# Kernel tuning notes

Hardware: AMD Instinct MI355X
Metric: run time of the kernel (lower is better)

## Reference

```python
import jax, jax.numpy as jnp
import numpy as np
import math

C = 512          # in_planes
H = 8            # num_heads
D = C // H       # head_dim = 64
EPS = 1e-12      # torch F.normalize eps


def _l2norm(x):
    # F.normalize(x, dim=-1): x / max(||x||_2, eps)
    n = jnp.sqrt(jnp.sum(x * x, axis=-1, keepdims=True))
    return x / jnp.maximum(n, EPS)


def setup_inputs() -> dict:
    key = jax.random.key(0)
    ks = jax.random.split(key, 8)
    q = jax.random.normal(ks[0], (8, 8, 256, C), dtype=jnp.float32)
    kv = jax.random.normal(ks[1], (8, 8, 512, C), dtype=jnp.float32)
    s = 0.02
    Wq = jax.random.normal(ks[2], (C, C), dtype=jnp.float32) * s
    bq = jax.random.normal(ks[3], (C,), dtype=jnp.float32) * s
    Wkv = jax.random.normal(ks[4], (2 * C, C), dtype=jnp.float32) * s
    bkv = jax.random.normal(ks[5], (2 * C,), dtype=jnp.float32) * s
    Wm = jax.random.normal(ks[6], (C, C), dtype=jnp.float32) * s
    bm = jax.random.normal(ks[7], (C,), dtype=jnp.float32) * s
    return {"q": q, "kv": kv, "Wq": Wq, "bq": bq, "Wkv": Wkv, "bkv": bkv, "Wm": Wm, "bm": bm}


def reference(q, kv, Wq, bq, Wkv, bkv, Wm, bm):
    b, t, lq, c = q.shape
    lk = kv.shape[2]
    shortcut = q

    # Q projection -> (b,t,h,lq,d), L2-normalized over d
    qh = (q @ Wq.T + bq).reshape(b, t, lq, H, D)
    qh = _l2norm(jnp.moveaxis(qh, 3, 2))  # (b,t,h,lq,d)

    # KV projection -> (b,t,2h,lk,d); first H heads = k, last H = v
    kvh = (kv @ Wkv.T + bkv).reshape(b, t, lk, 2 * H, D)
    kvh = jnp.moveaxis(kvh, 3, 2)          # (b,t,2h,lk,d)
    kh = _l2norm(kvh[:, :, :H])            # (b,t,h,lk,d)
    vh = _l2norm(kvh[:, :, H:])            # (b,t,h,lk,d)

    # cosine attention
    att = jnp.einsum('bthqd,bthkd->bthqk', qh, kh) / math.sqrt(D)
    att = jax.nn.softmax(att, axis=-1)
    x = jnp.einsum('bthqk,bthkd->bthqd', att, vh)  # (b,t,h,lq,d)

    # merge heads, output projection, residual
    x = jnp.moveaxis(x, 2, 3).reshape(b, t, lq, c)
    return x @ Wm.T + bm + shortcut
```

## Files before the change

### kernel.cpp

```cpp
#include <hip/hip_runtime.h>
#include <hip/hip_bf16.h>

using bf = __bf16;
typedef __attribute__((ext_vector_type(8))) __bf16 bf16x8;
typedef __attribute__((ext_vector_type(4))) float f32x4;

#define MFMA(a, b, c) __builtin_amdgcn_mfma_f32_16x16x32_bf16((a), (b), (c), 0, 0, 0)
#define GLL16(g, s)                                                         \
    __builtin_amdgcn_global_load_lds(                                       \
        (const __attribute__((address_space(1))) void*)(g),                 \
        (__attribute__((address_space(3))) void*)(s), 16, 0, 0)

static __device__ __forceinline__ void cvt_one(const float* __restrict__ s,
                                               bf* __restrict__ d, int i)
{
    const f32x4 a = ((const f32x4*)s)[2 * i];
    const f32x4 b = ((const f32x4*)s)[2 * i + 1];
    bf16x8 r;
#pragma unroll
    for (int k = 0; k < 4; ++k) { r[k] = (bf)a[k]; r[4 + k] = (bf)b[k]; }
    ((bf16x8*)d)[i] = r;
}

__global__ __launch_bounds__(256) void cvt2(const float* __restrict__ s1, bf* __restrict__ d1, int n1,
                                            const float* __restrict__ s2, bf* __restrict__ d2, int n2)
{
    int i = blockIdx.x * 256 + threadIdx.x;
    if (i < n1) { cvt_one(s1, d1, i); return; }
    i -= n1;
    if (i < n2) cvt_one(s2, d2, i);
}

__global__ __launch_bounds__(256) void cvt3(const float* __restrict__ s1, bf* __restrict__ d1, int n1,
                                            const float* __restrict__ s2, bf* __restrict__ d2, int n2,
                                            const float* __restrict__ s3, bf* __restrict__ d3, int n3)
{
    int i = blockIdx.x * 256 + threadIdx.x;
    if (i < n1) { cvt_one(s1, d1, i); return; }
    i -= n1;
    if (i < n2) { cvt_one(s2, d2, i); return; }
    i -= n2;
    if (i < n3) cvt_one(s3, d3, i);
}

template <int EPI, int GH, int LGR>
__global__ __launch_bounds__(256) void gemm128(
    const bf* __restrict__ A, const bf* __restrict__ W,
    const float* __restrict__ bias, const float* __restrict__ res,
    void* __restrict__ Cout, int M, int N, int K)
{
    __shared__ __attribute__((aligned(16))) bf As[128 * 32];
    __shared__ __attribute__((aligned(16))) bf Bs[128 * 32];

    const int lane = threadIdx.x & 63;
    const int wave = threadIdx.x >> 6;
    const int lm = lane & 15;
    const int quad = lane >> 4;
    const int row0 = blockIdx.x * 128, col0 = blockIdx.y * 128;
    const int wrow = (wave >> 1) * 64, wcol = (wave & 1) * 64;

    const int sr = lane >> 2;
    const int sc = (lane & 3) * 8;
    const bf* Ag = A + (size_t)(row0 + wave * 32 + sr) * K + sc;
    const bf* Wg = W + (size_t)(col0 + wave * 32 + sr) * K + sc;
    bf* AsW = As + wave * 1024;
    bf* BsW = Bs + wave * 1024;

    f32x4 acc[4][4] = {};

    for (int k0 = 0; k0 < K; k0 += 32) {
        GLL16(Ag + k0, AsW);
        GLL16(Ag + (size_t)16 * K + k0, AsW + 512);
        GLL16(Wg + k0, BsW);
        GLL16(Wg + (size_t)16 * K + k0, BsW + 512);
        __syncthreads();

        bf16x8 a[4], b[4];
#pragma unroll
        for (int i = 0; i < 4; ++i)
            a[i] = *(const bf16x8*)(As + (wrow + i * 16 + lm) * 32 + quad * 8);
#pragma unroll
        for (int j = 0; j < 4; ++j)
            b[j] = *(const bf16x8*)(Bs + (wcol + j * 16 + lm) * 32 + quad * 8);
#pragma unroll
        for (int i = 0; i < 4; ++i)
#pragma unroll
            for (int j = 0; j < 4; ++j)
                acc[i][j] = MFMA(a[i], b[j], acc[i][j]);
        __syncthreads();
    }

    float bv[4];
#pragma unroll
    for (int j = 0; j < 4; ++j) bv[j] = bias[col0 + wcol + j * 16 + lm];

    if (EPI == 0) {
        bf* C = (bf*)Cout;
        const int g = (col0 + wcol) >> 6;
#pragma unroll
        for (int i = 0; i < 4; ++i) {
#pragma unroll
            for (int rg = 0; rg < 4; ++rg) {
                float v[4];
                float ss = 0.f;
#pragma unroll
                for (int j = 0; j < 4; ++j) {
                    const float x = acc[i][j][rg] + bv[j];
                    v[j] = x;
                    ss += x * x;
                }
                ss += __shfl_xor(ss, 1, 64);
                ss += __shfl_xor(ss, 2, 64);
                ss += __shfl_xor(ss, 4, 64);
                ss += __shfl_xor(ss, 8, 64);
                const float inv = 1.0f / fmaxf(sqrtf(ss), 1e-12f);
                const int row = row0 + wrow + i * 16 + quad * 4 + rg;
                const int bt = row >> LGR;
                const int rl = row & ((1 << LGR) - 1);
                bf* Cr = C + (((size_t)(bt * GH + g) << LGR) + rl) * 64;
#pragma unroll
                for (int j = 0; j < 4; ++j)
                    Cr[j * 16 + lm] = (bf)(v[j] * inv);
            }
        }
    } else {
        float* C = (float*)Cout;
#pragma unroll
        for (int i = 0; i < 4; ++i) {
#pragma unroll
            for (int rg = 0; rg < 4; ++rg) {
                const int row = row0 + wrow + i * 16 + quad * 4 + rg;
#pragma unroll
                for (int j = 0; j < 4; ++j) {
                    const size_t idx = (size_t)row * N + col0 + wcol + j * 16 + lm;
                    C[idx] = acc[i][j][rg] + bv[j] + res[idx];
                }
            }
        }
    }
}

template <int GH, int LGR>
__global__ __launch_bounds__(512, 2) void gemm256(
    const bf* __restrict__ A, const bf* __restrict__ W,
    const float* __restrict__ bias, bf* __restrict__ C,
    int M, int N, int K)
{
    extern __shared__ __attribute__((aligned(16))) char smem[];
    char* Asm = smem;
    char* Bsm = smem + 65536;

    const int tid = threadIdx.x;
    const int lane = tid & 63;
    const int lm = lane & 15;
    const int quad = lane >> 4;
    const int wave = tid >> 6;
    const int wm = wave >> 2;
    const int wn = wave & 3;
    const int row0 = blockIdx.x * 256, col0 = blockIdx.y * 256;
    const int NT = K >> 6;

    const int trow = tid >> 3;
    const int tslot = (tid & 7) ^ (trow & 7);
    const bf* Ath = A + (size_t)(row0 + trow) * K + tslot * 8;
    const bf* Wth = W + (size_t)(col0 + trow) * K + tslot * 8;

    const char* aBase = Asm + wm * 16384 + lm * 128;
    const char* bBase = Bsm + (wn >> 1) * 16384 + ((wn & 1) * 64 + lm) * 128;
    const int skz0 = ((quad ^ (lm & 7)) << 4);
    const int skz1 = (((4 + quad) ^ (lm & 7)) << 4);

    f32x4 acc[8][4] = {};

    auto stA = [&](int kt) {
        const int bo = (kt & 1) * 32768;
#pragma unroll
        for (int h = 0; h < 2; ++h)
#pragma unroll
            for (int s = 0; s < 2; ++s)
                GLL16(Ath + (size_t)(h * 128 + s * 64) * K + kt * 64,
                      Asm + bo + h * 16384 + s * 8192 + tid * 16);
    };
    auto stB = [&](int kt) {
        const int bo = (kt & 1) * 32768;
#pragma unroll
        for (int h = 0; h < 2; ++h)
#pragma unroll
            for (int s = 0; s < 2; ++s)
                GLL16(Wth + (size_t)(h * 128 + s * 64) * K + kt * 64,
                      Bsm + bo + h * 16384 + s * 8192 + tid * 16);
    };

#define LOADA(bo, mh, kk)                                                     \
    _Pragma("unroll")                                                         \
    for (int mm = 0; mm < 4; ++mm)                                            \
        a[mm] = *(const bf16x8*)(aBase + (bo) + ((mh) * 4 + mm) * 2048        \
                                 + ((kk) ? skz1 : skz0));
#define LOADB(bo, kk)                                                         \
    _Pragma("unroll")                                                         \
    for (int j = 0; j < 4; ++j)                                               \
        b[j] = *(const bf16x8*)(bBase + (bo) + j * 2048                       \
                                + ((kk) ? skz1 : skz0));
#define PH_OPEN()                                                             \
    __builtin_amdgcn_s_barrier();                                             \
    asm volatile("s_waitcnt lgkmcnt(0)" ::: "memory");                        \
    __builtin_amdgcn_s_setprio(1)
#define MM16(mh)                                                              \
    _Pragma("unroll")                                                         \
    for (int mm = 0; mm < 4; ++mm)                                            \
        _Pragma("unroll")                                                     \
        for (int j = 0; j < 4; ++j)                                           \
            acc[(mh) * 4 + mm][j] = MFMA(a[mm], b[j], acc[(mh) * 4 + mm][j]);
#define PH_CLOSE()                                                            \
    __builtin_amdgcn_s_setprio(0);                                            \
    __builtin_amdgcn_s_barrier()

    stB(0); stA(0); stB(1);
    asm volatile("s_waitcnt vmcnt(4)" ::: "memory");
    __builtin_amdgcn_s_barrier();

    for (int it = 0; it < NT; it += 2) {
        const int more = (it + 2 < NT);
        bf16x8 a[4], b[4];

        LOADA(0, 0, 0) LOADB(0, 0) stA(it + 1);
        PH_OPEN(); MM16(0) PH_CLOSE();

        LOADA(0, 1, 0)
        PH_OPEN(); MM16(1) PH_CLOSE();

        LOADA(0, 0, 1) LOADB(0, 1)
        PH_OPEN(); MM16(0) PH_CLOSE();

        LOADA(0, 1, 1) if (more) stB(it + 2);
        PH_OPEN(); MM16(1)
        __builtin_amdgcn_s_setprio(0);
        if (more) { asm volatile("s_waitcnt vmcnt(4)" ::: "memory"); }
        else      { asm volatile("s_waitcnt vmcnt(0)" ::: "memory"); }
        __builtin_amdgcn_s_barrier();

        LOADA(32768, 0, 0) LOADB(32768, 0) if (more) stA(it + 2);
        PH_OPEN(); MM16(0) PH_CLOSE();

        LOADA(32768, 1, 0)
        PH_OPEN(); MM16(1) PH_CLOSE();

        LOADA(32768, 0, 1) LOADB(32768, 1)
        PH_OPEN(); MM16(0) PH_CLOSE();

        LOADA(32768, 1, 1) if (more) stB(it + 3);
        PH_OPEN(); MM16(1)
        __builtin_amdgcn_s_setprio(0);
        if (more) { asm volatile("s_waitcnt vmcnt(4)" ::: "memory"); }
        __builtin_amdgcn_s_barrier();
    }
#undef LOADA
#undef LOADB
#undef PH_OPEN
#undef MM16
#undef PH_CLOSE

    float bv[4];
#pragma unroll
    for (int j = 0; j < 4; ++j) bv[j] = bias[col0 + wn * 64 + j * 16 + lm];
    const int g = (col0 + wn * 64) >> 6;
#pragma unroll
    for (int m = 0; m < 8; ++m) {
#pragma unroll
        for (int rg = 0; rg < 4; ++rg) {
            float v[4];
            float ss = 0.f;
#pragma unroll
            for (int j = 0; j < 4; ++j) {
                const float x = acc[m][j][rg] + bv[j];
                v[j] = x;
                ss += x * x;
            }
            ss += __shfl_xor(ss, 1, 64);
            ss += __shfl_xor(ss, 2, 64);
            ss += __shfl_xor(ss, 4, 64);
            ss += __shfl_xor(ss, 8, 64);
            const float inv = 1.0f / fmaxf(sqrtf(ss), 1e-12f);
            const int row = row0 + wm * 128 + m * 16 + quad * 4 + rg;
            const int bt = row >> LGR;
            const int rl = row & ((1 << LGR) - 1);
            bf* Cr = C + (((size_t)(bt * GH + g) << LGR) + rl) * 64;
#pragma unroll
            for (int j = 0; j < 4; ++j)
                Cr[j * 16 + lm] = (bf)(v[j] * inv);
        }
    }
}

__global__ __launch_bounds__(256, 4) void attn(
    const bf* __restrict__ qn, const bf* __restrict__ kvn, bf* __restrict__ X)
{
    __shared__ __attribute__((aligned(16))) bf Kt[128 * 72];
    __shared__ __attribute__((aligned(16))) bf Vt[64 * 136];
    __shared__ __attribute__((aligned(16))) bf Ps[4][16 * 40];

    const int qb = blockIdx.x >> 9;
    const int rb = blockIdx.x & 511;
    const int bt = rb >> 3;
    const int h = rb & 7;
    const int tid = threadIdx.x;
    const int lane = tid & 63;
    const int wave = tid >> 6;
    const int lm = lane & 15;
    const int quad = lane >> 4;

    const bf* qh = qn + ((size_t)(bt * 8 + h) * 256 + qb * 128) * 64;
    const bf* kh = kvn + (size_t)(bt * 16 + h) * 512 * 64;
    const bf* vh = kvn + (size_t)(bt * 16 + 8 + h) * 512 * 64;

    const int srow = tid >> 1;
    const int sseg = (tid & 1) * 32;

    f32x4 o[2][4] = {};
    float sum[2][4] = {};
    bf* Pw = &Ps[wave][0];

    for (int t = 0; t < 4; ++t) {
        {
            const bf* kr = kh + (size_t)(t * 128 + srow) * 64 + sseg;
            bf* kd = Kt + srow * 72 + sseg;
#pragma unroll
            for (int j = 0; j < 4; ++j)
                *(bf16x8*)(kd + j * 8) = *(const bf16x8*)(kr + j * 8);

            const bf* vr = vh + (size_t)(t * 128 + srow) * 64 + sseg;
            bf16x8 vv[4];
#pragma unroll
            for (int j = 0; j < 4; ++j) vv[j] = *(const bf16x8*)(vr + j * 8);
#pragma unroll
            for (int j = 0; j < 4; ++j)
#pragma unroll
                for (int e = 0; e < 8; ++e)
                    Vt[(sseg + j * 8 + e) * 136 + srow] = vv[j][e];
        }
        __syncthreads();

#pragma unroll
        for (int c = 0; c < 2; ++c) {
            const int r0 = wave * 32 + c * 16;
            const bf* qp = qh + (size_t)(r0 + lm) * 64 + quad * 8;
            const bf16x8 a0 = *(const bf16x8*)qp;
            const bf16x8 a1 = *(const bf16x8*)(qp + 32);

            f32x4 s[8];
#pragma unroll
            for (int nt = 0; nt < 8; ++nt) {
                const bf16x8 k0 = *(const bf16x8*)(&Kt[(nt * 16 + lm) * 72 + quad * 8]);
                const bf16x8 k1 = *(const bf16x8*)(&Kt[(nt * 16 + lm) * 72 + 32 + quad * 8]);
                f32x4 z = {};
                z = MFMA(a0, k0, z);
                s[nt] = MFMA(a1, k1, z);
            }

            for (int ntp = 0; ntp < 4; ++ntp) {
#pragma unroll
                for (int tt = 0; tt < 2; ++tt)
#pragma unroll
                    for (int rr = 0; rr < 4; ++rr) {
                        const float e = __expf(s[ntp * 2 + tt][rr] * 0.125f);
                        sum[c][rr] += e;
                        Pw[(quad * 4 + rr) * 40 + tt * 16 + lm] = (bf)e;
                    }
                const bf16x8 ap = *(const bf16x8*)(&Pw[lm * 40 + quad * 8]);
#pragma unroll
                for (int dt = 0; dt < 4; ++dt) {
                    const bf16x8 bv = *(const bf16x8*)(&Vt[(dt * 16 + lm) * 136 + ntp * 32 + quad * 8]);
                    o[c][dt] = MFMA(ap, bv, o[c][dt]);
                }
            }
        }
        __syncthreads();
    }

#pragma unroll
    for (int c = 0; c < 2; ++c) {
        float inv[4];
#pragma unroll
        for (int rr = 0; rr < 4; ++rr) {
            float sm = sum[c][rr];
            sm += __shfl_xor(sm, 1, 64);
            sm += __shfl_xor(sm, 2, 64);
            sm += __shfl_xor(sm, 4, 64);
            sm += __shfl_xor(sm, 8, 64);
            inv[rr] = 1.0f / sm;
        }
        bf* Xp = X + ((size_t)bt * 256 + qb * 128 + wave * 32 + c * 16) * 512 + h * 64;
#pragma unroll
        for (int dt = 0; dt < 4; ++dt)
#pragma unroll
            for (int rr = 0; rr < 4; ++rr)
                Xp[(size_t)(quad * 4 + rr) * 512 + dt * 16 + lm] = (bf)(o[c][dt][rr] * inv[rr]);
    }
}

extern "C" void kernel_launch(void* const* d_in, const int* in_sizes, int n_in,
                              void* d_out, int out_size, void* d_ws, size_t ws_size,
                              hipStream_t stream)
{
    const float* q   = (const float*)d_in[0];
    const float* kv  = (const float*)d_in[1];
    const float* Wq  = (const float*)d_in[2];
    const float* bq  = (const float*)d_in[3];
    const float* Wkv = (const float*)d_in[4];
    const float* bkv = (const float*)d_in[5];
    const float* Wm  = (const float*)d_in[6];
    const float* bm  = (const float*)d_in[7];
    float* out = (float*)d_out;

    char* ws = (char*)d_ws;
    bf* kvb = (bf*)ws;
    bf* kvn = (bf*)(ws + (size_t)(32 << 20));
    bf* wqb = (bf*)ws;
    bf* wmb = (bf*)(ws + (size_t)(16 << 20));
    bf* X   = (bf*)ws;
    char* dob = (char*)d_out;
    bf* wkvb = (bf*)dob;
    bf* qb   = (bf*)dob;
    bf* qn   = (bf*)(dob + (size_t)(16 << 20));

    {
        auto k0 = gemm256<16, 9>;
        auto k1 = gemm256<8, 8>;
        (void)hipFuncSetAttribute((const void*)k0, hipFuncAttributeMaxDynamicSharedMemorySize, 131072);
        (void)hipFuncSetAttribute((const void*)k1, hipFuncAttributeMaxDynamicSharedMemorySize, 131072);
    }

    cvt2<<<dim3(8448), 256, 0, stream>>>(kv, kvb, 2097152, Wkv, wkvb, 65536);
    gemm256<16, 9><<<dim3(128, 4), 512, 131072, stream>>>(kvb, wkvb, bkv, kvn, 32768, 1024, 512);
    cvt3<<<dim3(4352), 256, 0, stream>>>(q, qb, 1048576, Wq, wqb, 32768, Wm, wmb, 32768);
    gemm256<8, 8><<<dim3(64, 2), 512, 131072, stream>>>(qb, wqb, bq, qn, 16384, 512, 512);
    attn<<<dim3(1024), 256, 0, stream>>>(qn, kvn, X);
    gemm128<1, 0, 0><<<dim3(128, 4), 256, 0, stream>>>(X, wmb, bm, q, out, 16384, 512, 512);
}
```

Measured before the change: 287.3 us.

## Fuse fp32-to-bf16 activation conversion into GEMM A-operand loads

Drops the separate conversion passes over kv and q and makes the projection GEMMs read fp32 activations directly. The KV gemm256 loads fp32 into registers a stage ahead and converts and writes swizzled bf16 to LDS, and the Q projection moves to gemm128 with an fp32 A path. This removes a full read-write round trip of the large activations through HBM. In exchange the A loads lose async global-to-LDS transfer, gain register pressure, and add conversion and LDS-store work inside the pipelined loop.

```diff
diff --git a/kernel.cpp b/kernel.cpp
--- a/kernel.cpp
+++ b/kernel.cpp
@@ -20,15 +20,6 @@
 #pragma unroll
     for (int k = 0; k < 4; ++k) { r[k] = (bf)a[k]; r[4 + k] = (bf)b[k]; }
     ((bf16x8*)d)[i] = r;
-}
-
-__global__ __launch_bounds__(256) void cvt2(const float* __restrict__ s1, bf* __restrict__ d1, int n1,
-                                            const float* __restrict__ s2, bf* __restrict__ d2, int n2)
-{
-    int i = blockIdx.x * 256 + threadIdx.x;
-    if (i < n1) { cvt_one(s1, d1, i); return; }
-    i -= n1;
-    if (i < n2) cvt_one(s2, d2, i);
 }
 
 __global__ __launch_bounds__(256) void cvt3(const float* __restrict__ s1, bf* __restrict__ d1, int n1,
@@ -43,9 +34,9 @@
     if (i < n3) cvt_one(s3, d3, i);
 }
 
-template <int EPI, int GH, int LGR>
+template <int EPI, int GH, int LGR, int AF32>
 __global__ __launch_bounds__(256) void gemm128(
-    const bf* __restrict__ A, const bf* __restrict__ W,
+    const void* __restrict__ Ap, const bf* __restrict__ W,
     const float* __restrict__ bias, const float* __restrict__ res,
     void* __restrict__ Cout, int M, int N, int K)
 {
@@ -61,7 +52,10 @@
 
     const int sr = lane >> 2;
     const int sc = (lane & 3) * 8;
-    const bf* Ag = A + (size_t)(row0 + wave * 32 + sr) * K + sc;
+    const bf* Ag = nullptr;
+    const float* Agf = nullptr;
+    if (AF32) Agf = (const float*)Ap + (size_t)(row0 + wave * 32 + sr) * K + sc;
+    else      Ag  = (const bf*)Ap + (size_t)(row0 + wave * 32 + sr) * K + sc;
     const bf* Wg = W + (size_t)(col0 + wave * 32 + sr) * K + sc;
     bf* AsW = As + wave * 1024;
     bf* BsW = Bs + wave * 1024;
@@ -69,8 +63,23 @@
     f32x4 acc[4][4] = {};
 
     for (int k0 = 0; k0 < K; k0 += 32) {
-        GLL16(Ag + k0, AsW);
-        GLL16(Ag + (size_t)16 * K + k0, AsW + 512);
+        if (AF32) {
+            f32x4 u0 = *(const f32x4*)(Agf + k0);
+            f32x4 u1 = *(const f32x4*)(Agf + k0 + 4);
+            f32x4 u2 = *(const f32x4*)(Agf + (size_t)16 * K + k0);
+            f32x4 u3 = *(const f32x4*)(Agf + (size_t)16 * K + k0 + 4);
+            bf16x8 r0, r1;
+#pragma unroll
+            for (int e = 0; e < 4; ++e) {
+                r0[e] = (bf)u0[e]; r0[4 + e] = (bf)u1[e];
+                r1[e] = (bf)u2[e]; r1[4 + e] = (bf)u3[e];
+            }
+            *(bf16x8*)(AsW + lane * 8) = r0;
+            *(bf16x8*)(AsW + 512 + lane * 8) = r1;
+        } else {
+            GLL16(Ag + k0, AsW);
+            GLL16(Ag + (size_t)16 * K + k0, AsW + 512);
+        }
         GLL16(Wg + k0, BsW);
         GLL16(Wg + (size_t)16 * K + k0, BsW + 512);
         __syncthreads();
@@ -142,7 +151,7 @@
 
 template <int GH, int LGR>
 __global__ __launch_bounds__(512, 2) void gemm256(
-    const bf* __restrict__ A, const bf* __restrict__ W,
+    const float* __restrict__ A, const bf* __restrict__ W,
     const float* __restrict__ bias, bf* __restrict__ C,
     int M, int N, int K)
 {
@@ -161,8 +170,10 @@
     const int NT = K >> 6;
 
     const int trow = tid >> 3;
-    const int tslot = (tid & 7) ^ (trow & 7);
-    const bf* Ath = A + (size_t)(row0 + trow) * K + tslot * 8;
+    const int slotL = tid & 7;
+    const int sphys = slotL ^ (trow & 7);
+    const int tslot = slotL ^ (trow & 7);
+    const float* Af = A + (size_t)(row0 + trow) * K + slotL * 8;
     const bf* Wth = W + (size_t)(col0 + trow) * K + tslot * 8;
 
     const char* aBase = Asm + wm * 16384 + lm * 128;
@@ -171,15 +182,28 @@
     const int skz1 = (((4 + quad) ^ (lm & 7)) << 4);
 
     f32x4 acc[8][4] = {};
-
-    auto stA = [&](int kt) {
+    f32x4 areg[4][2];
+
+    auto ldA = [&](int kt) {
+#pragma unroll
+        for (int hs = 0; hs < 4; ++hs) {
+            const float* p = Af + (size_t)((hs >> 1) * 128 + (hs & 1) * 64) * K + kt * 64;
+            areg[hs][0] = ((const f32x4*)p)[0];
+            areg[hs][1] = ((const f32x4*)p)[1];
+        }
+    };
+    auto wrA = [&](int kt) {
         const int bo = (kt & 1) * 32768;
 #pragma unroll
-        for (int h = 0; h < 2; ++h)
-#pragma unroll
-            for (int s = 0; s < 2; ++s)
-                GLL16(Ath + (size_t)(h * 128 + s * 64) * K + kt * 64,
-                      Asm + bo + h * 16384 + s * 8192 + tid * 16);
+        for (int hs = 0; hs < 4; ++hs) {
+            bf16x8 r;
+#pragma unroll
+            for (int e = 0; e < 4; ++e) {
+                r[e] = (bf)areg[hs][0][e];
+                r[4 + e] = (bf)areg[hs][1][e];
+            }
+            *(bf16x8*)(Asm + bo + (hs >> 1) * 16384 + (hs & 1) * 8192 + trow * 128 + sphys * 16) = r;
+        }
     };
     auto stB = [&](int kt) {
         const int bo = (kt & 1) * 32768;
@@ -215,15 +239,17 @@
     __builtin_amdgcn_s_setprio(0);                                            \
     __builtin_amdgcn_s_barrier()
 
-    stB(0); stA(0); stB(1);
+    stB(0); ldA(0); stB(1);
     asm volatile("s_waitcnt vmcnt(4)" ::: "memory");
+    wrA(0);
+    asm volatile("s_waitcnt lgkmcnt(0)" ::: "memory");
     __builtin_amdgcn_s_barrier();
 
     for (int it = 0; it < NT; it += 2) {
         const int more = (it + 2 < NT);
         bf16x8 a[4], b[4];
 
-        LOADA(0, 0, 0) LOADB(0, 0) stA(it + 1);
+        LOADA(0, 0, 0) LOADB(0, 0) ldA(it + 1);
         PH_OPEN(); MM16(0) PH_CLOSE();
 
         LOADA(0, 1, 0)
@@ -237,9 +263,11 @@
         __builtin_amdgcn_s_setprio(0);
         if (more) { asm volatile("s_waitcnt vmcnt(4)" ::: "memory"); }
         else      { asm volatile("s_waitcnt vmcnt(0)" ::: "memory"); }
+        wrA(it + 1);
+        asm volatile("s_waitcnt lgkmcnt(0)" ::: "memory");
         __builtin_amdgcn_s_barrier();
 
-        LOADA(32768, 0, 0) LOADB(32768, 0) if (more) stA(it + 2);
+        LOADA(32768, 0, 0) LOADB(32768, 0) if (more) ldA(it + 2);
         PH_OPEN(); MM16(0) PH_CLOSE();
 
         LOADA(32768, 1, 0)
@@ -251,7 +279,11 @@
         LOADA(32768, 1, 1) if (more) stB(it + 3);
         PH_OPEN(); MM16(1)
         __builtin_amdgcn_s_setprio(0);
-        if (more) { asm volatile("s_waitcnt vmcnt(4)" ::: "memory"); }
+        if (more) {
+            asm volatile("s_waitcnt vmcnt(4)" ::: "memory");
+            wrA(it + 2);
+            asm volatile("s_waitcnt lgkmcnt(0)" ::: "memory");
+        }
         __builtin_amdgcn_s_barrier();
     }
 #undef LOADA
@@ -413,27 +445,21 @@
     float* out = (float*)d_out;
 
     char* ws = (char*)d_ws;
-    bf* kvb = (bf*)ws;
-    bf* kvn = (bf*)(ws + (size_t)(32 << 20));
-    bf* wqb = (bf*)ws;
-    bf* wmb = (bf*)(ws + (size_t)(16 << 20));
-    bf* X   = (bf*)ws;
-    char* dob = (char*)d_out;
-    bf* wkvb = (bf*)dob;
-    bf* qb   = (bf*)dob;
-    bf* qn   = (bf*)(dob + (size_t)(16 << 20));
+    bf* kvn  = (bf*)ws;
+    bf* wqb  = (bf*)(ws + ((size_t)64 << 20));
+    bf* wkvb = (bf*)(ws + ((size_t)64 << 20) + ((size_t)512 << 10));
+    bf* wmb  = (bf*)(ws + ((size_t)65 << 20) + ((size_t)512 << 10));
+    bf* X    = (bf*)(ws + ((size_t)66 << 20));
+    bf* qn   = (bf*)d_out;
 
     {
         auto k0 = gemm256<16, 9>;
-        auto k1 = gemm256<8, 8>;
         (void)hipFuncSetAttribute((const void*)k0, hipFuncAttributeMaxDynamicSharedMemorySize, 131072);
-        (void)hipFuncSetAttribute((const void*)k1, hipFuncAttributeMaxDynamicSharedMemorySize, 131072);
-    }
-
-    cvt2<<<dim3(8448), 256, 0, stream>>>(kv, kvb, 2097152, Wkv, wkvb, 65536);
-    gemm256<16, 9><<<dim3(128, 4), 512, 131072, stream>>>(kvb, wkvb, bkv, kvn, 32768, 1024, 512);
-    cvt3<<<dim3(4352), 256, 0, stream>>>(q, qb, 1048576, Wq, wqb, 32768, Wm, wmb, 32768);
-    gemm256<8, 8><<<dim3(64, 2), 512, 131072, stream>>>(qb, wqb, bq, qn, 16384, 512, 512);
+    }
+
+    cvt3<<<dim3(512), 256, 0, stream>>>(Wq, wqb, 32768, Wkv, wkvb, 65536, Wm, wmb, 32768);
+    gemm256<16, 9><<<dim3(128, 4), 512, 131072, stream>>>(kv, wkvb, bkv, kvn, 32768, 1024, 512);
+    gemm128<0, 8, 8, 1><<<dim3(128, 4), 256, 0, stream>>>(q, wqb, bq, nullptr, qn, 16384, 512, 512);
     attn<<<dim3(1024), 256, 0, stream>>>(qn, kvn, X);
-    gemm128<1, 0, 0><<<dim3(128, 4), 256, 0, stream>>>(X, wmb, bm, q, out, 16384, 512, 512);
-}
+    gemm128<1, 0, 0, 0><<<dim3(128, 4), 256, 0, stream>>>(X, wmb, bm, q, out, 16384, 512, 512);
+}
```

After: 295.7 us. 2.9% more time.

## Fuse fp32-to-bf16 conversion into GEMM loads and merge Q projection with KV cast

Applied to the files above, without the earlier changes.

The separate cvt3 pass and the Q-projection GEMM are removed. The Q projection now runs in a 128-tile GEMM that reads fp32 q and Wq directly and converts them to bf16 while staging into LDS, and it shares one launch with the kv/Wkv conversion blocks. The output projection likewise reads fp32 Wm directly. This drops the intermediate bf16 buffers and two launches. In exchange the fused loads are plain register loads plus conversions rather than async global-to-LDS copies, and the Q GEMM uses a smaller tile than before.

```diff
diff --git a/kernel.cpp b/kernel.cpp
--- a/kernel.cpp
+++ b/kernel.cpp
@@ -22,32 +22,11 @@
     ((bf16x8*)d)[i] = r;
 }
 
-__global__ __launch_bounds__(256) void cvt2(const float* __restrict__ s1, bf* __restrict__ d1, int n1,
-                                            const float* __restrict__ s2, bf* __restrict__ d2, int n2)
-{
-    int i = blockIdx.x * 256 + threadIdx.x;
-    if (i < n1) { cvt_one(s1, d1, i); return; }
-    i -= n1;
-    if (i < n2) cvt_one(s2, d2, i);
-}
-
-__global__ __launch_bounds__(256) void cvt3(const float* __restrict__ s1, bf* __restrict__ d1, int n1,
-                                            const float* __restrict__ s2, bf* __restrict__ d2, int n2,
-                                            const float* __restrict__ s3, bf* __restrict__ d3, int n3)
-{
-    int i = blockIdx.x * 256 + threadIdx.x;
-    if (i < n1) { cvt_one(s1, d1, i); return; }
-    i -= n1;
-    if (i < n2) { cvt_one(s2, d2, i); return; }
-    i -= n2;
-    if (i < n3) cvt_one(s3, d3, i);
-}
-
-template <int EPI, int GH, int LGR>
-__global__ __launch_bounds__(256) void gemm128(
-    const bf* __restrict__ A, const bf* __restrict__ W,
+template <int EPI, int GH, int LGR, int AF32, int BF32>
+static __device__ __forceinline__ void gemm128_body(
+    const void* __restrict__ Ap, const void* __restrict__ Wp,
     const float* __restrict__ bias, const float* __restrict__ res,
-    void* __restrict__ Cout, int M, int N, int K)
+    void* __restrict__ Cout, int bx, int by, int N, int K)
 {
     __shared__ __attribute__((aligned(16))) bf As[128 * 32];
     __shared__ __attribute__((aligned(16))) bf Bs[128 * 32];
@@ -56,23 +35,57 @@
     const int wave = threadIdx.x >> 6;
     const int lm = lane & 15;
     const int quad = lane >> 4;
-    const int row0 = blockIdx.x * 128, col0 = blockIdx.y * 128;
+    const int row0 = bx * 128, col0 = by * 128;
     const int wrow = (wave >> 1) * 64, wcol = (wave & 1) * 64;
 
     const int sr = lane >> 2;
     const int sc = (lane & 3) * 8;
-    const bf* Ag = A + (size_t)(row0 + wave * 32 + sr) * K + sc;
-    const bf* Wg = W + (size_t)(col0 + wave * 32 + sr) * K + sc;
+    const bf* Ag = nullptr; const float* Agf = nullptr;
+    if (AF32) Agf = (const float*)Ap + (size_t)(row0 + wave * 32 + sr) * K + sc;
+    else      Ag  = (const bf*)Ap + (size_t)(row0 + wave * 32 + sr) * K + sc;
+    const bf* Wg = nullptr; const float* Wgf = nullptr;
+    if (BF32) Wgf = (const float*)Wp + (size_t)(col0 + wave * 32 + sr) * K + sc;
+    else      Wg  = (const bf*)Wp + (size_t)(col0 + wave * 32 + sr) * K + sc;
     bf* AsW = As + wave * 1024;
     bf* BsW = Bs + wave * 1024;
 
     f32x4 acc[4][4] = {};
 
     for (int k0 = 0; k0 < K; k0 += 32) {
-        GLL16(Ag + k0, AsW);
-        GLL16(Ag + (size_t)16 * K + k0, AsW + 512);
-        GLL16(Wg + k0, BsW);
-        GLL16(Wg + (size_t)16 * K + k0, BsW + 512);
+        if (AF32) {
+            f32x4 u0 = *(const f32x4*)(Agf + k0);
+            f32x4 u1 = *(const f32x4*)(Agf + k0 + 4);
+            f32x4 u2 = *(const f32x4*)(Agf + (size_t)16 * K + k0);
+            f32x4 u3 = *(const f32x4*)(Agf + (size_t)16 * K + k0 + 4);
+            bf16x8 r0, r1;
+#pragma unroll
+            for (int e = 0; e < 4; ++e) {
+                r0[e] = (bf)u0[e]; r0[4 + e] = (bf)u1[e];
+                r1[e] = (bf)u2[e]; r1[4 + e] = (bf)u3[e];
+            }
+            *(bf16x8*)(AsW + lane * 8) = r0;
+            *(bf16x8*)(AsW + 512 + lane * 8) = r1;
+        } else {
+            GLL16(Ag + k0, AsW);
+            GLL16(Ag + (size_t)16 * K + k0, AsW + 512);
+        }
+        if (BF32) {
+            f32x4 w0 = *(const f32x4*)(Wgf + k0);
+            f32x4 w1 = *(const f32x4*)(Wgf + k0 + 4);
+            f32x4 w2 = *(const f32x4*)(Wgf + (size_t)16 * K + k0);
+            f32x4 w3 = *(const f32x4*)(Wgf + (size_t)16 * K + k0 + 4);
+            bf16x8 s0, s1;
+#pragma unroll
+            for (int e = 0; e < 4; ++e) {
+                s0[e] = (bf)w0[e]; s0[4 + e] = (bf)w1[e];
+                s1[e] = (bf)w2[e]; s1[4 + e] = (bf)w3[e];
+            }
+            *(bf16x8*)(BsW + lane * 8) = s0;
+            *(bf16x8*)(BsW + 512 + lane * 8) = s1;
+        } else {
+            GLL16(Wg + k0, BsW);
+            GLL16(Wg + (size_t)16 * K + k0, BsW + 512);
+        }
         __syncthreads();
 
         bf16x8 a[4], b[4];
@@ -140,11 +153,35 @@
     }
 }
 
-template <int GH, int LGR>
-__global__ __launch_bounds__(512, 2) void gemm256(
+__global__ __launch_bounds__(256) void proj_cvt(
+    const float* __restrict__ q, const float* __restrict__ Wq,
+    const float* __restrict__ bq, bf* __restrict__ qn,
+    const float* __restrict__ kv, bf* __restrict__ kvb,
+    const float* __restrict__ Wkv, bf* __restrict__ wkvb)
+{
+    const int bx = blockIdx.x;
+    if (bx < 512) {
+        gemm128_body<0, 8, 8, 1, 1>(q, Wq, bq, nullptr, qn, bx & 127, bx >> 7, 512, 512);
+        return;
+    }
+    int i = (bx - 512) * 256 + threadIdx.x;
+    if (i < 2097152) { cvt_one(kv, kvb, i); return; }
+    i -= 2097152;
+    if (i < 65536) cvt_one(Wkv, wkvb, i);
+}
+
+__global__ __launch_bounds__(256) void outproj(
+    const bf* __restrict__ X, const float* __restrict__ Wm,
+    const float* __restrict__ bm, const float* __restrict__ q,
+    float* __restrict__ out)
+{
+    gemm128_body<1, 0, 0, 0, 1>(X, Wm, bm, q, out, blockIdx.x, blockIdx.y, 512, 512);
+}
+
+static __device__ __forceinline__ void gemm256_body(
     const bf* __restrict__ A, const bf* __restrict__ W,
     const float* __restrict__ bias, bf* __restrict__ C,
-    int M, int N, int K)
+    const int bxx, const int byy, const int K)
 {
     extern __shared__ __attribute__((aligned(16))) char smem[];
     char* Asm = smem;
@@ -157,13 +194,14 @@
     const int wave = tid >> 6;
     const int wm = wave >> 2;
     const int wn = wave & 3;
-    const int row0 = blockIdx.x * 256, col0 = blockIdx.y * 256;
+    const int row0 = bxx * 256, col0 = byy * 256;
     const int NT = K >> 6;
 
     const int trow = tid >> 3;
-    const int tslot = (tid & 7) ^ (trow & 7);
-    const bf* Ath = A + (size_t)(row0 + trow) * K + tslot * 8;
-    const bf* Wth = W + (size_t)(col0 + trow) * K + tslot * 8;
+    const int slotL = tid & 7;
+    const int sswz = slotL ^ (trow & 7);
+    const bf* Ab  = A + (size_t)(row0 + trow) * K + sswz * 8;
+    const bf* Wth = W + (size_t)(col0 + trow) * K + sswz * 8;
 
     const char* aBase = Asm + wm * 16384 + lm * 128;
     const char* bBase = Bsm + (wn >> 1) * 16384 + ((wn & 1) * 64 + lm) * 128;
@@ -178,7 +216,7 @@
         for (int h = 0; h < 2; ++h)
 #pragma unroll
             for (int s = 0; s < 2; ++s)
-                GLL16(Ath + (size_t)(h * 128 + s * 64) * K + kt * 64,
+                GLL16(Ab + (size_t)(h * 128 + s * 64) * K + kt * 64,
                       Asm + bo + h * 16384 + s * 8192 + tid * 16);
     };
     auto stB = [&](int kt) {
@@ -282,14 +320,22 @@
             ss += __shfl_xor(ss, 8, 64);
             const float inv = 1.0f / fmaxf(sqrtf(ss), 1e-12f);
             const int row = row0 + wm * 128 + m * 16 + quad * 4 + rg;
-            const int bt = row >> LGR;
-            const int rl = row & ((1 << LGR) - 1);
-            bf* Cr = C + (((size_t)(bt * GH + g) << LGR) + rl) * 64;
+            const int bt = row >> 9;
+            const int rl = row & 511;
+            bf* Cr = C + (((size_t)(bt * 16 + g) << 9) + rl) * 64;
 #pragma unroll
             for (int j = 0; j < 4; ++j)
                 Cr[j * 16 + lm] = (bf)(v[j] * inv);
         }
     }
+}
+
+__global__ __launch_bounds__(512, 2) void gemm256kv(
+    const bf* __restrict__ kvb, const bf* __restrict__ wkvb,
+    const float* __restrict__ bkv, bf* __restrict__ kvn)
+{
+    const int b = blockIdx.x;
+    gemm256_body(kvb, wkvb, bkv, kvn, b & 127, b >> 7, 512);
 }
 
 __global__ __launch_bounds__(256, 4) void attn(
@@ -414,26 +460,17 @@
 
     char* ws = (char*)d_ws;
     bf* kvb = (bf*)ws;
-    bf* kvn = (bf*)(ws + (size_t)(32 << 20));
-    bf* wqb = (bf*)ws;
-    bf* wmb = (bf*)(ws + (size_t)(16 << 20));
+    bf* kvn = (bf*)(ws + ((size_t)32 << 20));
     bf* X   = (bf*)ws;
     char* dob = (char*)d_out;
     bf* wkvb = (bf*)dob;
-    bf* qb   = (bf*)dob;
-    bf* qn   = (bf*)(dob + (size_t)(16 << 20));
-
-    {
-        auto k0 = gemm256<16, 9>;
-        auto k1 = gemm256<8, 8>;
-        (void)hipFuncSetAttribute((const void*)k0, hipFuncAttributeMaxDynamicSharedMemorySize, 131072);
-        (void)hipFuncSetAttribute((const void*)k1, hipFuncAttributeMaxDynamicSharedMemorySize, 131072);
-    }
-
-    cvt2<<<dim3(8448), 256, 0, stream>>>(kv, kvb, 2097152, Wkv, wkvb, 65536);
-    gemm256<16, 9><<<dim3(128, 4), 512, 131072, stream>>>(kvb, wkvb, bkv, kvn, 32768, 1024, 512);
-    cvt3<<<dim3(4352), 256, 0, stream>>>(q, qb, 1048576, Wq, wqb, 32768, Wm, wmb, 32768);
-    gemm256<8, 8><<<dim3(64, 2), 512, 131072, stream>>>(qb, wqb, bq, qn, 16384, 512, 512);
+    bf* qn   = (bf*)(dob + ((size_t)16 << 20));
+
+    (void)hipFuncSetAttribute((const void*)gemm256kv,
+                              hipFuncAttributeMaxDynamicSharedMemorySize, 131072);
+
+    proj_cvt<<<dim3(8960), 256, 0, stream>>>(q, Wq, bq, qn, kv, kvb, Wkv, wkvb);
+    gemm256kv<<<dim3(512), 512, 131072, stream>>>(kvb, wkvb, bkv, kvn);
     attn<<<dim3(1024), 256, 0, stream>>>(qn, kvn, X);
-    gemm128<1, 0, 0><<<dim3(128, 4), 256, 0, stream>>>(X, wmb, bm, q, out, 16384, 512, 512);
-}
+    outproj<<<dim3(128, 4), 256, 0, stream>>>(X, Wm, bm, q, out);
+}
```

New measurement: 289.2 us. No clear change (+0.7%).
